# Kernel tuning notes

Measured on AMD Instinct MI355X. Metric: run time of the kernel, lower is better.

## Reference

```python
import jax, jax.numpy as jnp
import numpy as np

HEADS = 24
HEAD_DIM = 128
DIM = HEADS * HEAD_DIM  # 3072
EPS = 1e-5


def _rms_norm(x, w):
    # x: [B,S,H,D], w: [D]
    var = jnp.mean(jnp.square(x), axis=-1, keepdims=True)
    return x * jax.lax.rsqrt(var + EPS) * w


def _apply_rope(x, cos, sin):
    # non-neox (interleaved pairs): x: [B,S,H,D], cos/sin: [S,D]
    B, S, H, D = x.shape
    xr = x.reshape(B, S, H, D // 2, 2)
    x_real, x_imag = xr[..., 0], xr[..., 1]
    rotated = jnp.stack([-x_imag, x_real], axis=-1).reshape(B, S, H, D)
    c = cos[None, :, None, :]
    s = sin[None, :, None, :]
    return x * c + rotated * s


def setup_inputs() -> dict:
    key = jax.random.key(0)
    ks = jax.random.split(key, 20)
    B, S_img, S_txt = 1, 2048, 512
    S = S_img + S_txt
    sc = 1.0 / np.sqrt(DIM)
    inp = {
        "x": jax.random.normal(ks[0], (B, S_img, DIM), jnp.float32),
        "encoder_hidden_states": jax.random.normal(ks[1], (B, S_txt, DIM), jnp.float32),
        "rope_cos": jax.random.uniform(ks[2], (S, HEAD_DIM), jnp.float32),
        "rope_sin": jax.random.uniform(ks[3], (S, HEAD_DIM), jnp.float32),
        # image-stream projections (bias=False)
        "wq": jax.random.normal(ks[4], (DIM, DIM), jnp.float32) * sc,
        "wk": jax.random.normal(ks[5], (DIM, DIM), jnp.float32) * sc,
        "wv": jax.random.normal(ks[6], (DIM, DIM), jnp.float32) * sc,
        # text-stream projections (added_proj_bias=True)
        "w_add_q": jax.random.normal(ks[7], (DIM, DIM), jnp.float32) * sc,
        "w_add_k": jax.random.normal(ks[8], (DIM, DIM), jnp.float32) * sc,
        "w_add_v": jax.random.normal(ks[9], (DIM, DIM), jnp.float32) * sc,
        "b_add_q": jax.random.normal(ks[10], (DIM,), jnp.float32) * 0.01,
        "b_add_k": jax.random.normal(ks[11], (DIM,), jnp.float32) * 0.01,
        "b_add_v": jax.random.normal(ks[12], (DIM,), jnp.float32) * 0.01,
        # per-head RMSNorm weights
        "norm_q_w": jnp.ones((HEAD_DIM,), jnp.float32),
        "norm_k_w": jnp.ones((HEAD_DIM,), jnp.float32),
        "norm_aq_w": jnp.ones((HEAD_DIM,), jnp.float32),
        "norm_ak_w": jnp.ones((HEAD_DIM,), jnp.float32),
        # output projections (out_bias=True)
        "w_out": jax.random.normal(ks[13], (DIM, DIM), jnp.float32) * sc,
        "b_out": jax.random.normal(ks[14], (DIM,), jnp.float32) * 0.01,
        "w_add_out": jax.random.normal(ks[15], (DIM, DIM), jnp.float32) * sc,
        "b_add_out": jax.random.normal(ks[16], (DIM,), jnp.float32) * 0.01,
    }
    return inp


def reference(x, encoder_hidden_states, rope_cos, rope_sin,
              wq, wk, wv, w_add_q, w_add_k, w_add_v,
              b_add_q, b_add_k, b_add_v,
              norm_q_w, norm_k_w, norm_aq_w, norm_ak_w,
              w_out, b_out, w_add_out, b_add_out):
    B, S_img, _ = x.shape
    S_txt = encoder_hidden_states.shape[1]

    def proj(h, w, b=None):
        y = jnp.einsum('bsd,ed->bse', h, w)
        return y if b is None else y + b

    def heads(t):
        return t.reshape(B, t.shape[1], HEADS, HEAD_DIM)

    q = _rms_norm(heads(proj(x, wq)), norm_q_w)
    k = _rms_norm(heads(proj(x, wk)), norm_k_w)
    v = heads(proj(x, wv))

    eq = _rms_norm(heads(proj(encoder_hidden_states, w_add_q, b_add_q)), norm_aq_w)
    ek = _rms_norm(heads(proj(encoder_hidden_states, w_add_k, b_add_k)), norm_ak_w)
    ev = heads(proj(encoder_hidden_states, w_add_v, b_add_v))

    # encoder tokens first, then image tokens
    q = jnp.concatenate([eq, q], axis=1)
    k = jnp.concatenate([ek, k], axis=1)
    v = jnp.concatenate([ev, v], axis=1)

    q = _apply_rope(q, rope_cos, rope_sin)
    k = _apply_rope(k, rope_cos, rope_sin)

    scale = 1.0 / np.sqrt(HEAD_DIM)
    scores = jnp.einsum('bqhd,bkhd->bhqk', q, k) * scale
    attn = jax.nn.softmax(scores, axis=-1)
    o = jnp.einsum('bhqk,bkhd->bqhd', attn, v)
    o = o.reshape(B, S_txt + S_img, DIM)

    enc_o, img_o = o[:, :S_txt], o[:, S_txt:]
    img_out = jnp.einsum('bsd,ed->bse', img_o, w_out) + b_out
    enc_out = jnp.einsum('bsd,ed->bse', enc_o, w_add_out) + b_add_out
    return img_out, enc_out
```

## Files before the change

kernel.cpp:

```cpp
#include <hip/hip_runtime.h>
#include <hip/hip_bf16.h>


typedef __hip_bfloat16 bf16;
typedef __attribute__((ext_vector_type(8))) short short8;
typedef __attribute__((ext_vector_type(4))) short s16x4;
typedef __attribute__((ext_vector_type(4))) float f32x4;

#define KDIM 3072
#define S_TXT 512
#define S_IMG 2048
#define S_ALL 2560
#define NHEADS 24
#define HDIM 128
#define WELEM (KDIM * KDIM)
#define AELEM (S_ALL * KDIM)
#define NSPLIT 3
#define NT_K 48

__device__ __forceinline__ void async_ld16(const void* g, void* l) {
  __builtin_amdgcn_global_load_lds((__attribute__((address_space(1))) void*)g,
                                   (__attribute__((address_space(3))) void*)l,
                                   16, 0, 0);
}

__device__ __forceinline__ short bf16_bits(float x) {
  bf16 h = (bf16)x;
  return __builtin_bit_cast(short, h);
}
__device__ __forceinline__ float bits_f32(short s) {
  return (float)__builtin_bit_cast(bf16, s);
}

__device__ __forceinline__ void phase_mid() {
  __builtin_amdgcn_s_barrier();
  asm volatile("s_waitcnt lgkmcnt(0)" ::: "memory");
  __builtin_amdgcn_sched_barrier(0);
  __builtin_amdgcn_s_setprio(1);
}
__device__ __forceinline__ void phase_end() {
  __builtin_amdgcn_s_setprio(0);
  __builtin_amdgcn_s_barrier();
}

__global__ __launch_bounds__(256) void cast_weights_kernel(
    const float* __restrict__ w0, const float* __restrict__ w1,
    const float* __restrict__ w2, const float* __restrict__ w3,
    const float* __restrict__ w4, const float* __restrict__ w5,
    const float* __restrict__ w6, const float* __restrict__ w7,
    bf16* __restrict__ dst) {
  const float* srcs[8] = {w0, w1, w2, w3, w4, w5, w6, w7};
  const float* __restrict__ src = srcs[blockIdx.y];
  bf16* __restrict__ out = dst + (size_t)blockIdx.y * WELEM;
  const size_t i0 = ((size_t)blockIdx.x * 256 + threadIdx.x) * 8;
  const float4 f0 = *(const float4*)(src + i0);
  const float4 f1 = *(const float4*)(src + i0 + 4);
  short8 o;
  o[0] = bf16_bits(f0.x); o[1] = bf16_bits(f0.y);
  o[2] = bf16_bits(f0.z); o[3] = bf16_bits(f0.w);
  o[4] = bf16_bits(f1.x); o[5] = bf16_bits(f1.y);
  o[6] = bf16_bits(f1.z); o[7] = bf16_bits(f1.w);
  *(short8*)(out + i0) = o;
}

__global__ __launch_bounds__(256) void cast_acts_kernel(
    const float* __restrict__ x, const float* __restrict__ enc,
    bf16* __restrict__ xe) {
  const size_t i0 = ((size_t)blockIdx.x * 256 + threadIdx.x) * 8;
  const size_t TXT = (size_t)S_TXT * KDIM;
  const float* __restrict__ src = (i0 < TXT) ? (enc + i0) : (x + (i0 - TXT));
  const float4 f0 = *(const float4*)(src);
  const float4 f1 = *(const float4*)(src + 4);
  short8 o;
  o[0] = bf16_bits(f0.x); o[1] = bf16_bits(f0.y);
  o[2] = bf16_bits(f0.z); o[3] = bf16_bits(f0.w);
  o[4] = bf16_bits(f1.x); o[5] = bf16_bits(f1.y);
  o[6] = bf16_bits(f1.z); o[7] = bf16_bits(f1.w);
  *(short8*)(xe + i0) = o;
}

template <typename OutT, bool TRANS>
__device__ __forceinline__ void gemm256(const bf16* __restrict__ Ab,
                                        const bf16* __restrict__ Bb,
                                        OutT* __restrict__ C,
                                        const float* __restrict__ bias,
                                        short* sAmem, short* sBmem) {
  const int tid = threadIdx.x;
  const int lane = tid & 63;
  const int w = tid >> 6;
  const int a = lane & 15;
  const int g = (lane >> 4) & 3;
  const int wm = w >> 2;
  const int wn = w & 3;

  short* const A00 = sAmem;
  short* const A01 = sAmem + 8192;
  short* const A10 = sAmem + 16384;
  short* const A11 = sAmem + 24576;
  short* const B00 = sBmem;
  short* const B01 = sBmem + 8192;
  short* const B10 = sBmem + 16384;
  short* const B11 = sBmem + 24576;

  auto stage = [&](const bf16* gb, int kbase, short* lblk) {
#pragma unroll
    for (int l = 0; l < 2; l++) {
      const int t = l * 512 + tid;
      const int row = t >> 2;
      const int ls = (t & 3) ^ ((row >> 1) & 3);
      async_ld16(gb + (size_t)row * KDIM + kbase + ls * 8,
                 lblk + (l * 512 + w * 64) * 8);
    }
  };
  auto frag = [&](const short* lblk, int R) -> short8 {
    return *(const short8*)(lblk + R * 32 + ((g ^ ((R >> 1) & 3)) * 8));
  };

  f32x4 acc[8][4] = {};

  stage(Bb, 0, B00);
  stage(Ab, 0, A00);
  stage(Bb, 32, B01);
  stage(Ab, 32, A01);
  stage(Bb, 64, B10);
  stage(Ab, 64, A10);
  stage(Bb, 96, B11);
  asm volatile("s_waitcnt vmcnt(6)" ::: "memory");
  __builtin_amdgcn_s_barrier();

  const int ra = wm * 128 + a;
  const int rb = wn * 64 + a;

  auto kblock = [&](int u, short* cA0, short* cA1, short* cB0, short* cB1,
                    short* nA1) {
    short8 af[4], bfr[4];
#pragma unroll
    for (int i = 0; i < 4; i++) af[i] = frag(cA0, ra + i * 16);
#pragma unroll
    for (int j = 0; j < 4; j++) bfr[j] = frag(cB0, rb + j * 16);
    if (u + 1 < NT_K) stage(Ab, (u + 1) * 64 + 32, nA1);
    phase_mid();
#pragma unroll
    for (int i = 0; i < 4; i++)
#pragma unroll
      for (int j = 0; j < 4; j++)
        acc[i][j] = __builtin_amdgcn_mfma_f32_16x16x32_bf16(af[i], bfr[j], acc[i][j], 0, 0, 0);
    phase_end();
#pragma unroll
    for (int i = 0; i < 4; i++) af[i] = frag(cA0, ra + (i + 4) * 16);
    if (u + 2 < NT_K) stage(Bb, (u + 2) * 64, cB0);
    phase_mid();
#pragma unroll
    for (int i = 0; i < 4; i++)
#pragma unroll
      for (int j = 0; j < 4; j++)
        acc[i + 4][j] = __builtin_amdgcn_mfma_f32_16x16x32_bf16(af[i], bfr[j], acc[i + 4][j], 0, 0, 0);
    phase_end();
#pragma unroll
    for (int i = 0; i < 4; i++) af[i] = frag(cA1, ra + i * 16);
#pragma unroll
    for (int j = 0; j < 4; j++) bfr[j] = frag(cB1, rb + j * 16);
    if (u + 2 < NT_K) stage(Ab, (u + 2) * 64, cA0);
    phase_mid();
#pragma unroll
    for (int i = 0; i < 4; i++)
#pragma unroll
      for (int j = 0; j < 4; j++)
        acc[i][j] = __builtin_amdgcn_mfma_f32_16x16x32_bf16(af[i], bfr[j], acc[i][j], 0, 0, 0);
    phase_end();
#pragma unroll
    for (int i = 0; i < 4; i++) af[i] = frag(cA1, ra + (i + 4) * 16);
    if (u + 2 < NT_K) stage(Bb, (u + 2) * 64 + 32, cB1);
    __builtin_amdgcn_s_barrier();
    asm volatile("s_waitcnt lgkmcnt(0)" ::: "memory");
    __builtin_amdgcn_sched_barrier(0);
    __builtin_amdgcn_s_setprio(1);
#pragma unroll
    for (int i = 0; i < 4; i++)
#pragma unroll
      for (int j = 0; j < 4; j++)
        acc[i + 4][j] = __builtin_amdgcn_mfma_f32_16x16x32_bf16(af[i], bfr[j], acc[i + 4][j], 0, 0, 0);
    __builtin_amdgcn_s_setprio(0);
    if (u < NT_K - 2)
      asm volatile("s_waitcnt vmcnt(6)" ::: "memory");
    else
      asm volatile("s_waitcnt vmcnt(0)" ::: "memory");
    __builtin_amdgcn_s_barrier();
  };

#pragma unroll 1
  for (int u = 0; u < NT_K; u += 2) {
    kblock(u,     A00, A01, B00, B01, A11);
    kblock(u + 1, A10, A11, B10, B11, A01);
  }

  if constexpr (TRANS) {
#pragma unroll
    for (int i = 0; i < 8; i++)
#pragma unroll
      for (int j = 0; j < 4; j++) {
        const int col = wn * 64 + j * 16 + a;
        const float bv = bias ? bias[col] : 0.0f;
        s16x4 pk;
#pragma unroll
        for (int r = 0; r < 4; r++) pk[r] = bf16_bits(acc[i][j][r] + bv);
        *(s16x4*)((short*)C + (size_t)col * S_ALL + wm * 128 + i * 16 + g * 4) = pk;
      }
  } else {
#pragma unroll
    for (int i = 0; i < 8; i++)
#pragma unroll
      for (int j = 0; j < 4; j++) {
        const int col = wn * 64 + j * 16 + a;
        const float bv = bias ? bias[col] : 0.0f;
#pragma unroll
        for (int r = 0; r < 4; r++) {
          const int row = wm * 128 + i * 16 + g * 4 + r;
          C[(size_t)row * KDIM + col] = (OutT)(acc[i][j][r] + bv);
        }
      }
  }
}

__global__ __launch_bounds__(512, 2) void qkv_kernel(
    const bf16* __restrict__ XE, const bf16* __restrict__ Wc,
    const float* __restrict__ bq, const float* __restrict__ bk, const float* __restrict__ bv,
    bf16* __restrict__ Q, bf16* __restrict__ K, bf16* __restrict__ VT) {
  __shared__ alignas(16) short sAmem[4 * 8192];
  __shared__ alignas(16) short sBmem[4 * 8192];
  const int bid = blockIdx.x;
  const int wk_ = (bid & 7) * 45 + (bid >> 3);
  const int bm = wk_ / 36;
  const int bn = wk_ % 36;
  const int which = bn / 12;
  const int nc = (bn % 12) * 256;
  const bool txt = bm < 2;
  const bf16* W = Wc + (size_t)(txt ? (3 + which) : which) * WELEM + (size_t)nc * KDIM;
  const float* bias = nullptr;
  if (txt) bias = ((which == 0) ? bq : (which == 1) ? bk : bv) + nc;
  const int crow = bm * 256;
  const bf16* A = XE + (size_t)crow * KDIM;
  if (which == 2) {
    gemm256<bf16, true>(A, W, VT + (size_t)nc * S_ALL + crow, bias, sAmem, sBmem);
  } else {
    bf16* Out = (which == 0) ? Q : K;
    gemm256<bf16, false>(A, W, Out + (size_t)crow * KDIM + nc, bias, sAmem, sBmem);
  }
}

template <typename OutT, bool TRANS>
__device__ __forceinline__ void gemm_tile(const bf16* __restrict__ A,
                                          const bf16* __restrict__ B,
                                          OutT* __restrict__ C,
                                          const float* __restrict__ bias) {
  __shared__ alignas(16) short sA[128 * 32];
  __shared__ alignas(16) short sB[128 * 32];
  const int tid = threadIdx.x;
  const int lane = tid & 63;
  const int w = tid >> 6;
  const int a = lane & 15;
  const int g = lane >> 4;
  const int wm = (w >> 1) * 64;
  const int wn = (w & 1) * 64;

  f32x4 acc[4][4] = {};

  const int s0 = tid, s1 = tid + 256;
  const int r0 = s0 >> 2, b0 = (s0 & 3) ^ ((r0 >> 1) & 3);
  const int r1 = s1 >> 2, b1 = (s1 & 3) ^ ((r1 >> 1) & 3);
  const bf16* gA0 = A + (size_t)r0 * KDIM + b0 * 8;
  const bf16* gA1 = A + (size_t)r1 * KDIM + b1 * 8;
  const bf16* gB0 = B + (size_t)r0 * KDIM + b0 * 8;
  const bf16* gB1 = B + (size_t)r1 * KDIM + b1 * 8;
  short* lA0 = sA + (w * 64) * 8;
  short* lA1 = sA + (256 + w * 64) * 8;
  short* lB0 = sB + (w * 64) * 8;
  short* lB1 = sB + (256 + w * 64) * 8;

  for (int k0 = 0; k0 < KDIM; k0 += 32) {
    __syncthreads();
    async_ld16(gA0 + k0, lA0);
    async_ld16(gA1 + k0, lA1);
    async_ld16(gB0 + k0, lB0);
    async_ld16(gB1 + k0, lB1);
    __syncthreads();
    short8 af[4], bfg[4];
#pragma unroll
    for (int i = 0; i < 4; i++) {
      const int R = wm + i * 16 + a;
      af[i] = *(const short8*)(sA + R * 32 + ((g ^ ((R >> 1) & 3)) * 8));
    }
#pragma unroll
    for (int j = 0; j < 4; j++) {
      const int R = wn + j * 16 + a;
      bfg[j] = *(const short8*)(sB + R * 32 + ((g ^ ((R >> 1) & 3)) * 8));
    }
#pragma unroll
    for (int i = 0; i < 4; i++)
#pragma unroll
      for (int j = 0; j < 4; j++)
        acc[i][j] = __builtin_amdgcn_mfma_f32_16x16x32_bf16(af[i], bfg[j], acc[i][j], 0, 0, 0);
  }

  if constexpr (TRANS) {
#pragma unroll
    for (int i = 0; i < 4; i++)
#pragma unroll
      for (int j = 0; j < 4; j++) {
        const int col = wn + j * 16 + a;
        const float bv = bias ? bias[col] : 0.0f;
        s16x4 pk;
#pragma unroll
        for (int r = 0; r < 4; r++) pk[r] = bf16_bits(acc[i][j][r] + bv);
        *(s16x4*)((short*)C + (size_t)col * S_ALL + wm + i * 16 + g * 4) = pk;
      }
  } else {
#pragma unroll
    for (int i = 0; i < 4; i++)
#pragma unroll
      for (int j = 0; j < 4; j++) {
        const int col = wn + j * 16 + a;
        const float bv = bias ? bias[col] : 0.0f;
#pragma unroll
        for (int r = 0; r < 4; r++) {
          const int row = wm + i * 16 + g * 4 + r;
          C[(size_t)row * KDIM + col] = (OutT)(acc[i][j][r] + bv);
        }
      }
  }
}

__global__ __launch_bounds__(256) void outproj_kernel(
    const bf16* __restrict__ Obuf, const bf16* __restrict__ Wc,
    const float* __restrict__ b_out, const float* __restrict__ b_add,
    float* __restrict__ out) {
  const int bm = blockIdx.x;
  const int bn = blockIdx.y;
  const bool txt = bm < 4;
  const bf16* A = Obuf + (size_t)bm * 128 * KDIM;
  const bf16* W = Wc + (size_t)(txt ? 7 : 6) * WELEM;
  const float* bias = txt ? b_add : b_out;
  float* C = txt ? (out + (size_t)S_IMG * KDIM + (size_t)bm * 128 * KDIM)
                 : (out + (size_t)(bm - 4) * 128 * KDIM);
  gemm_tile<float, false>(A, W + (size_t)bn * 128 * KDIM, C + bn * 128, bias + bn * 128);
}

__global__ __launch_bounds__(256) void norm_rope_kernel(
    bf16* __restrict__ Q, bf16* __restrict__ K,
    const float* __restrict__ rc, const float* __restrict__ rs,
    const float* __restrict__ nqw, const float* __restrict__ nkw,
    const float* __restrict__ naqw, const float* __restrict__ nakw) {
  const int row = blockIdx.x;
  const int h = blockIdx.y * 4 + (threadIdx.x >> 6);
  const int t = threadIdx.x & 63;
  const long base = (long)row * KDIM + h * HDIM;
  const int d0 = 2 * t, d1 = d0 + 1;
  const bool txt = row < S_TXT;
  const float QSCL = 0.08838834764831845f * 1.4426950408889634f;
  float qa = (float)Q[base + d0], qb = (float)Q[base + d1];
  float ka = (float)K[base + d0], kb = (float)K[base + d1];
  float sq = qa * qa + qb * qb;
  float sk = ka * ka + kb * kb;
#pragma unroll
  for (int m = 1; m < 64; m <<= 1) {
    sq += __shfl_xor(sq, m);
    sk += __shfl_xor(sk, m);
  }
  const float rq = rsqrtf(sq * (1.0f / 128.0f) + 1e-5f) * QSCL;
  const float rk = rsqrtf(sk * (1.0f / 128.0f) + 1e-5f);
  const float* qw = txt ? naqw : nqw;
  const float* kw = txt ? nakw : nkw;
  const float c0 = rc[row * HDIM + d0], c1 = rc[row * HDIM + d1];
  const float s0 = rs[row * HDIM + d0], s1 = rs[row * HDIM + d1];
  const float qn0 = qa * rq * qw[d0], qn1 = qb * rq * qw[d1];
  const float kn0 = ka * rk * kw[d0], kn1 = kb * rk * kw[d1];
  Q[base + d0] = (bf16)(qn0 * c0 - qn1 * s0);
  Q[base + d1] = (bf16)(qn1 * c1 + qn0 * s1);
  K[base + d0] = (bf16)(kn0 * c0 - kn1 * s0);
  K[base + d1] = (bf16)(kn1 * c1 + kn0 * s1);
}

__global__ __launch_bounds__(256) void flash_kernel(
    const bf16* __restrict__ Q, const bf16* __restrict__ Kb,
    const bf16* __restrict__ VT,
    bf16* __restrict__ Op0, bf16* __restrict__ Op1, bf16* __restrict__ Op2,
    float* __restrict__ L) {
  __shared__ alignas(16) short sK[64 * 128];
  __shared__ alignas(16) short sVT[128 * 64];
  __shared__ alignas(16) short sP[4][32 * 72];
  const int tid = threadIdx.x;
  const int lane = tid & 63;
  const int w = tid >> 6;
  const int a = lane & 15;
  const int g = lane >> 4;
  const int qt = blockIdx.x;
  const int h = blockIdx.y;
  const int split = blockIdx.z;
  const int it0 = split * 13;
  const int it1 = (split == 2) ? 40 : (it0 + 13);
  const int qrow0 = qt * 128 + w * 32;
  short* const sPw = sP[w];

  short8 qf[2][4];
#pragma unroll
  for (int mi = 0; mi < 2; mi++)
#pragma unroll
    for (int kk = 0; kk < 4; kk++)
      qf[mi][kk] = *(const short8*)(Q + (size_t)(qrow0 + mi * 16 + a) * KDIM + h * HDIM + kk * 32 + g * 8);

  f32x4 oacc[2][8] = {};
  float lsum[2] = {0.0f, 0.0f};

  for (int it = it0; it < it1; ++it) {
    const int kv0 = it * 64;
    __syncthreads();
#pragma unroll
    for (int is = 0; is < 4; is++) {
      const int s = is * 256 + w * 64 + lane;
      const int kr = s >> 4, p = s & 15;
      const int lb = (p - (kr & 7)) & 15;
      async_ld16(Kb + (size_t)(kv0 + kr) * KDIM + h * HDIM + lb * 8,
                 sK + (is * 256 + w * 64) * 8);
    }
#pragma unroll
    for (int is = 0; is < 4; is++) {
      const int s = is * 256 + w * 64 + lane;
      const int dr = s >> 3, p = s & 7;
      const int lb = (p - (dr & 7)) & 7;
      async_ld16(VT + (size_t)(h * HDIM + dr) * S_ALL + kv0 + lb * 8,
                 sVT + (is * 256 + w * 64) * 8);
    }
    __syncthreads();

    f32x4 st[4][2] = {};
#pragma unroll
    for (int kk = 0; kk < 4; kk++) {
      short8 kf[4];
#pragma unroll
      for (int ni = 0; ni < 4; ni++) {
        const int kr = ni * 16 + a;
        const int p = ((kk * 4 + g) + (kr & 7)) & 15;
        kf[ni] = *(const short8*)(sK + kr * 128 + p * 8);
      }
#pragma unroll
      for (int ni = 0; ni < 4; ni++)
#pragma unroll
        for (int mi = 0; mi < 2; mi++)
          st[ni][mi] = __builtin_amdgcn_mfma_f32_16x16x32_bf16(kf[ni], qf[mi][kk], st[ni][mi], 0, 0, 0);
    }

#pragma unroll
    for (int mi = 0; mi < 2; mi++)
#pragma unroll
      for (int ni = 0; ni < 4; ni++) {
        s16x4 pk;
#pragma unroll
        for (int r = 0; r < 4; r++) {
          const float p = exp2f(st[ni][mi][r]);
          lsum[mi] += p;
          pk[r] = bf16_bits(p);
        }
        *(s16x4*)(sPw + (mi * 16 + a) * 72 + ni * 16 + g * 4) = pk;
      }

#pragma unroll
    for (int ks = 0; ks < 2; ks++) {
      short8 pf[2];
#pragma unroll
      for (int mi = 0; mi < 2; mi++)
        pf[mi] = *(const short8*)(sPw + (mi * 16 + a) * 72 + ks * 32 + g * 8);
#pragma unroll
      for (int nd = 0; nd < 8; nd++) {
        const int dr = nd * 16 + a;
        const int p = ((ks * 4 + g) + (dr & 7)) & 7;
        const short8 vf = *(const short8*)(sVT + dr * 64 + p * 8);
#pragma unroll
        for (int mi = 0; mi < 2; mi++)
          oacc[mi][nd] = __builtin_amdgcn_mfma_f32_16x16x32_bf16(pf[mi], vf, oacc[mi][nd], 0, 0, 0);
      }
    }
  }

#pragma unroll
  for (int mi = 0; mi < 2; mi++) {
    lsum[mi] += __shfl_xor(lsum[mi], 16);
    lsum[mi] += __shfl_xor(lsum[mi], 32);
  }
  bf16* __restrict__ Op = (split == 0) ? Op0 : (split == 1) ? Op1 : Op2;
#pragma unroll
  for (int mi = 0; mi < 2; mi++) {
#pragma unroll
    for (int r = 0; r < 4; r++) {
      const float inv = 1.0f / __shfl(lsum[mi], g * 4 + r);
      const size_t row = qrow0 + mi * 16 + g * 4 + r;
#pragma unroll
      for (int nd = 0; nd < 8; nd++)
        Op[row * KDIM + h * HDIM + nd * 16 + a] = (bf16)(oacc[mi][nd][r] * inv);
    }
    if (g == 0)
      L[((size_t)split * NHEADS + h) * S_ALL + qrow0 + mi * 16 + a] = lsum[mi];
  }
}

__global__ __launch_bounds__(256) void merge_kernel(
    bf16* __restrict__ O0, const bf16* __restrict__ O1, const bf16* __restrict__ O2,
    const float* __restrict__ L) {
  const size_t i0 = ((size_t)blockIdx.x * 256 + threadIdx.x) * 8;
  const int row = (int)(i0 / KDIM);
  const int h = (int)((i0 % KDIM) >> 7);
  const float l0 = L[((size_t)0 * NHEADS + h) * S_ALL + row];
  const float l1 = L[((size_t)1 * NHEADS + h) * S_ALL + row];
  const float l2 = L[((size_t)2 * NHEADS + h) * S_ALL + row];
  const float inv = 1.0f / (l0 + l1 + l2);
  const float w0 = l0 * inv, w1 = l1 * inv, w2 = l2 * inv;
  const short8 v0 = *(const short8*)(O0 + i0);
  const short8 v1 = *(const short8*)(O1 + i0);
  const short8 v2 = *(const short8*)(O2 + i0);
  short8 o;
#pragma unroll
  for (int u = 0; u < 8; u++)
    o[u] = bf16_bits(w0 * bits_f32(v0[u]) + w1 * bits_f32(v1[u]) + w2 * bits_f32(v2[u]));
  *(short8*)(O0 + i0) = o;
}

extern "C" void kernel_launch(void* const* d_in, const int* in_sizes, int n_in,
                              void* d_out, int out_size, void* d_ws, size_t ws_size,
                              hipStream_t stream) {
  const float* x    = (const float*)d_in[0];
  const float* enc  = (const float*)d_in[1];
  const float* rc   = (const float*)d_in[2];
  const float* rs   = (const float*)d_in[3];
  const float* wq   = (const float*)d_in[4];
  const float* wk   = (const float*)d_in[5];
  const float* wv   = (const float*)d_in[6];
  const float* waq  = (const float*)d_in[7];
  const float* wak  = (const float*)d_in[8];
  const float* wav  = (const float*)d_in[9];
  const float* bq   = (const float*)d_in[10];
  const float* bk   = (const float*)d_in[11];
  const float* bv   = (const float*)d_in[12];
  const float* nqw  = (const float*)d_in[13];
  const float* nkw  = (const float*)d_in[14];
  const float* naqw = (const float*)d_in[15];
  const float* nakw = (const float*)d_in[16];
  const float* w_out     = (const float*)d_in[17];
  const float* b_out     = (const float*)d_in[18];
  const float* w_add_out = (const float*)d_in[19];
  const float* b_add_out = (const float*)d_in[20];

  bf16* Wc   = (bf16*)d_ws;
  bf16* XE   = Wc + (size_t)8 * WELEM;
  bf16* Q    = XE + AELEM;
  bf16* K    = Q + AELEM;
  bf16* VT   = K + AELEM;
  bf16* Obuf = VT + AELEM;
  bf16* Op1  = Obuf + AELEM;
  bf16* Op2  = XE;
  float* L   = (float*)(Op1 + AELEM);

  cast_weights_kernel<<<dim3(WELEM / 2048, 8), 256, 0, stream>>>(
      wq, wk, wv, waq, wak, wav, w_out, w_add_out, Wc);
  cast_acts_kernel<<<dim3(AELEM / 2048), 256, 0, stream>>>(x, enc, XE);

  qkv_kernel<<<dim3(360), dim3(512), 0, stream>>>(XE, Wc, bq, bk, bv, Q, K, VT);
  norm_rope_kernel<<<dim3(S_ALL, 6), 256, 0, stream>>>(Q, K, rc, rs, nqw, nkw, naqw, nakw);
  flash_kernel<<<dim3(20, NHEADS, NSPLIT), 256, 0, stream>>>(Q, K, VT, Obuf, Op1, Op2, L);
  merge_kernel<<<dim3(AELEM / 2048), 256, 0, stream>>>(Obuf, Op1, Op2, L);
  outproj_kernel<<<dim3(20, NHEADS), 256, 0, stream>>>(Obuf, Wc, b_out, b_add_out,
                                                       (float*)d_out);
}
```

Measured before the change: 754.3 us.

## Retile QKV GEMM to 256x192 tiles with 4x2 wave layout

The QKV projection GEMM tile changes from 256x256 to 256x192. Waves are rearranged to 4x2, each computing 64x96, and the grid grows from 360 to 480 blocks. The B staging, LDS buffers and the vmcnt counts in the software pipeline are reworked to match. The aim is better wave quantization across the CUs and less LDS use per block, at the cost of lower arithmetic intensity per tile and more redundant loads of A.

```diff
diff --git a/kernel.cpp b/kernel.cpp
--- a/kernel.cpp
+++ b/kernel.cpp
@@ -17,6 +17,7 @@
 #define AELEM (S_ALL * KDIM)
 #define NSPLIT 3
 #define NT_K 48
+#define QBN 192
 
 __device__ __forceinline__ void async_ld16(const void* g, void* l) {
   __builtin_amdgcn_global_load_lds((__attribute__((address_space(1))) void*)g,
@@ -90,87 +91,104 @@
   const int w = tid >> 6;
   const int a = lane & 15;
   const int g = (lane >> 4) & 3;
-  const int wm = w >> 2;
-  const int wn = w & 3;
+  const int wm = w >> 1;
+  const int wn = w & 1;
 
   short* const A00 = sAmem;
   short* const A01 = sAmem + 8192;
   short* const A10 = sAmem + 16384;
   short* const A11 = sAmem + 24576;
   short* const B00 = sBmem;
-  short* const B01 = sBmem + 8192;
-  short* const B10 = sBmem + 16384;
-  short* const B11 = sBmem + 24576;
-
-  auto stage = [&](const bf16* gb, int kbase, short* lblk) {
+  short* const B01 = sBmem + 6144;
+  short* const B10 = sBmem + 12288;
+  short* const B11 = sBmem + 18432;
+
+  auto stageA = [&](int kbase, short* lblk) {
 #pragma unroll
     for (int l = 0; l < 2; l++) {
       const int t = l * 512 + tid;
       const int row = t >> 2;
       const int ls = (t & 3) ^ ((row >> 1) & 3);
-      async_ld16(gb + (size_t)row * KDIM + kbase + ls * 8,
+      async_ld16(Ab + (size_t)row * KDIM + kbase + ls * 8,
                  lblk + (l * 512 + w * 64) * 8);
+    }
+  };
+  auto stageB = [&](int kbase, short* lblk) {
+    {
+      const int t = tid;
+      const int row = t >> 2;
+      const int ls = (t & 3) ^ ((row >> 1) & 3);
+      async_ld16(Bb + (size_t)row * KDIM + kbase + ls * 8,
+                 lblk + (w * 64) * 8);
+    }
+    if (w < 4) {
+      const int t = 512 + tid;
+      const int row = t >> 2;
+      const int ls = (t & 3) ^ ((row >> 1) & 3);
+      async_ld16(Bb + (size_t)row * KDIM + kbase + ls * 8,
+                 lblk + (512 + w * 64) * 8);
     }
   };
   auto frag = [&](const short* lblk, int R) -> short8 {
     return *(const short8*)(lblk + R * 32 + ((g ^ ((R >> 1) & 3)) * 8));
   };
 
-  f32x4 acc[8][4] = {};
-
-  stage(Bb, 0, B00);
-  stage(Ab, 0, A00);
-  stage(Bb, 32, B01);
-  stage(Ab, 32, A01);
-  stage(Bb, 64, B10);
-  stage(Ab, 64, A10);
-  stage(Bb, 96, B11);
-  asm volatile("s_waitcnt vmcnt(6)" ::: "memory");
+  f32x4 acc[4][6] = {};
+
+  stageB(0, B00);
+  stageA(0, A00);
+  stageB(32, B01);
+  stageA(32, A01);
+  stageA(64, A10);
+  stageB(64, B10);
+  asm volatile("s_waitcnt vmcnt(3)" ::: "memory");
   __builtin_amdgcn_s_barrier();
 
-  const int ra = wm * 128 + a;
-  const int rb = wn * 64 + a;
+  const int ra = wm * 64 + a;
+  const int rb = wn * 96 + a;
 
   auto kblock = [&](int u, short* cA0, short* cA1, short* cB0, short* cB1,
-                    short* nA1) {
-    short8 af[4], bfr[4];
+                    short* nA1, short* nB1) {
+    short8 af[4], bfr[3];
 #pragma unroll
     for (int i = 0; i < 4; i++) af[i] = frag(cA0, ra + i * 16);
 #pragma unroll
-    for (int j = 0; j < 4; j++) bfr[j] = frag(cB0, rb + j * 16);
-    if (u + 1 < NT_K) stage(Ab, (u + 1) * 64 + 32, nA1);
+    for (int j = 0; j < 3; j++) bfr[j] = frag(cB0, rb + j * 16);
+    if (u + 1 < NT_K) {
+      stageA((u + 1) * 64 + 32, nA1);
+      stageB((u + 1) * 64 + 32, nB1);
+    }
     phase_mid();
 #pragma unroll
     for (int i = 0; i < 4; i++)
 #pragma unroll
-      for (int j = 0; j < 4; j++)
+      for (int j = 0; j < 3; j++)
         acc[i][j] = __builtin_amdgcn_mfma_f32_16x16x32_bf16(af[i], bfr[j], acc[i][j], 0, 0, 0);
     phase_end();
 #pragma unroll
-    for (int i = 0; i < 4; i++) af[i] = frag(cA0, ra + (i + 4) * 16);
-    if (u + 2 < NT_K) stage(Bb, (u + 2) * 64, cB0);
+    for (int j = 0; j < 3; j++) bfr[j] = frag(cB0, rb + (j + 3) * 16);
+    if (u + 2 < NT_K) stageA((u + 2) * 64, cA0);
     phase_mid();
 #pragma unroll
     for (int i = 0; i < 4; i++)
 #pragma unroll
-      for (int j = 0; j < 4; j++)
-        acc[i + 4][j] = __builtin_amdgcn_mfma_f32_16x16x32_bf16(af[i], bfr[j], acc[i + 4][j], 0, 0, 0);
+      for (int j = 0; j < 3; j++)
+        acc[i][j + 3] = __builtin_amdgcn_mfma_f32_16x16x32_bf16(af[i], bfr[j], acc[i][j + 3], 0, 0, 0);
     phase_end();
 #pragma unroll
     for (int i = 0; i < 4; i++) af[i] = frag(cA1, ra + i * 16);
 #pragma unroll
-    for (int j = 0; j < 4; j++) bfr[j] = frag(cB1, rb + j * 16);
-    if (u + 2 < NT_K) stage(Ab, (u + 2) * 64, cA0);
+    for (int j = 0; j < 3; j++) bfr[j] = frag(cB1, rb + j * 16);
+    if (u + 2 < NT_K) stageB((u + 2) * 64, cB0);
     phase_mid();
 #pragma unroll
     for (int i = 0; i < 4; i++)
 #pragma unroll
-      for (int j = 0; j < 4; j++)
+      for (int j = 0; j < 3; j++)
         acc[i][j] = __builtin_amdgcn_mfma_f32_16x16x32_bf16(af[i], bfr[j], acc[i][j], 0, 0, 0);
     phase_end();
 #pragma unroll
-    for (int i = 0; i < 4; i++) af[i] = frag(cA1, ra + (i + 4) * 16);
-    if (u + 2 < NT_K) stage(Bb, (u + 2) * 64 + 32, cB1);
+    for (int j = 0; j < 3; j++) bfr[j] = frag(cB1, rb + (j + 3) * 16);
     __builtin_amdgcn_s_barrier();
     asm volatile("s_waitcnt lgkmcnt(0)" ::: "memory");
     __builtin_amdgcn_sched_barrier(0);
@@ -178,11 +196,11 @@
 #pragma unroll
     for (int i = 0; i < 4; i++)
 #pragma unroll
-      for (int j = 0; j < 4; j++)
-        acc[i + 4][j] = __builtin_amdgcn_mfma_f32_16x16x32_bf16(af[i], bfr[j], acc[i + 4][j], 0, 0, 0);
+      for (int j = 0; j < 3; j++)
+        acc[i][j + 3] = __builtin_amdgcn_mfma_f32_16x16x32_bf16(af[i], bfr[j], acc[i][j + 3], 0, 0, 0);
     __builtin_amdgcn_s_setprio(0);
     if (u < NT_K - 2)
-      asm volatile("s_waitcnt vmcnt(6)" ::: "memory");
+      asm volatile("s_waitcnt vmcnt(3)" ::: "memory");
     else
       asm volatile("s_waitcnt vmcnt(0)" ::: "memory");
     __builtin_amdgcn_s_barrier();
@@ -190,32 +208,32 @@
 
 #pragma unroll 1
   for (int u = 0; u < NT_K; u += 2) {
-    kblock(u,     A00, A01, B00, B01, A11);
-    kblock(u + 1, A10, A11, B10, B11, A01);
+    kblock(u,     A00, A01, B00, B01, A11, B11);
+    kblock(u + 1, A10, A11, B10, B11, A01, B01);
   }
 
   if constexpr (TRANS) {
 #pragma unroll
-    for (int i = 0; i < 8; i++)
-#pragma unroll
-      for (int j = 0; j < 4; j++) {
-        const int col = wn * 64 + j * 16 + a;
+    for (int i = 0; i < 4; i++)
+#pragma unroll
+      for (int j = 0; j < 6; j++) {
+        const int col = wn * 96 + j * 16 + a;
         const float bv = bias ? bias[col] : 0.0f;
         s16x4 pk;
 #pragma unroll
         for (int r = 0; r < 4; r++) pk[r] = bf16_bits(acc[i][j][r] + bv);
-        *(s16x4*)((short*)C + (size_t)col * S_ALL + wm * 128 + i * 16 + g * 4) = pk;
+        *(s16x4*)((short*)C + (size_t)col * S_ALL + wm * 64 + i * 16 + g * 4) = pk;
       }
   } else {
 #pragma unroll
-    for (int i = 0; i < 8; i++)
-#pragma unroll
-      for (int j = 0; j < 4; j++) {
-        const int col = wn * 64 + j * 16 + a;
+    for (int i = 0; i < 4; i++)
+#pragma unroll
+      for (int j = 0; j < 6; j++) {
+        const int col = wn * 96 + j * 16 + a;
         const float bv = bias ? bias[col] : 0.0f;
 #pragma unroll
         for (int r = 0; r < 4; r++) {
-          const int row = wm * 128 + i * 16 + g * 4 + r;
+          const int row = wm * 64 + i * 16 + g * 4 + r;
           C[(size_t)row * KDIM + col] = (OutT)(acc[i][j][r] + bv);
         }
       }
@@ -227,13 +245,13 @@
     const float* __restrict__ bq, const float* __restrict__ bk, const float* __restrict__ bv,
     bf16* __restrict__ Q, bf16* __restrict__ K, bf16* __restrict__ VT) {
   __shared__ alignas(16) short sAmem[4 * 8192];
-  __shared__ alignas(16) short sBmem[4 * 8192];
+  __shared__ alignas(16) short sBmem[4 * 6144];
   const int bid = blockIdx.x;
-  const int wk_ = (bid & 7) * 45 + (bid >> 3);
-  const int bm = wk_ / 36;
-  const int bn = wk_ % 36;
-  const int which = bn / 12;
-  const int nc = (bn % 12) * 256;
+  const int wk_ = (bid & 7) * 60 + (bid >> 3);
+  const int bm = wk_ / 48;
+  const int bn = wk_ % 48;
+  const int which = bn / 16;
+  const int nc = (bn % 16) * QBN;
   const bool txt = bm < 2;
   const bf16* W = Wc + (size_t)(txt ? (3 + which) : which) * WELEM + (size_t)nc * KDIM;
   const float* bias = nullptr;
@@ -562,7 +580,7 @@
       wq, wk, wv, waq, wak, wav, w_out, w_add_out, Wc);
   cast_acts_kernel<<<dim3(AELEM / 2048), 256, 0, stream>>>(x, enc, XE);
 
-  qkv_kernel<<<dim3(360), dim3(512), 0, stream>>>(XE, Wc, bq, bk, bv, Q, K, VT);
+  qkv_kernel<<<dim3(480), dim3(512), 0, stream>>>(XE, Wc, bq, bk, bv, Q, K, VT);
   norm_rope_kernel<<<dim3(S_ALL, 6), 256, 0, stream>>>(Q, K, rc, rs, nqw, nkw, naqw, nakw);
   flash_kernel<<<dim3(20, NHEADS, NSPLIT), 256, 0, stream>>>(Q, K, VT, Obuf, Op1, Op2, L);
   merge_kernel<<<dim3(AELEM / 2048), 256, 0, stream>>>(Obuf, Op1, Op2, L);
```

Measured after the change: 738.5 us. -2.1%, faster.
